# Optimization experiments

Measured on AMD Instinct MI355X. Metric: run time of the kernel, lower is better.

Reference implementation:

```python
import jax, jax.numpy as jnp
import numpy as np

N_NODES = 50000
N_EDGES = 600000
IN_DIM, HID, OUT_DIM = 128, 128, 64
LN_EPS = 1e-5


def setup_inputs() -> dict:
    key = jax.random.key(0)
    ks = jax.random.split(key, 10)
    def glorot(k, shape):
        lim = np.sqrt(6.0 / (shape[0] + shape[1]))
        return jax.random.uniform(k, shape, jnp.float32, -lim, lim)
    return {
        "x": jax.random.normal(ks[0], (N_NODES, IN_DIM), jnp.float32),
        "src": jax.random.randint(ks[1], (N_EDGES,), 0, N_NODES, jnp.int32),
        "dst": jax.random.randint(ks[2], (N_EDGES,), 0, N_NODES, jnp.int32),
        "W0": glorot(ks[3], (IN_DIM, HID)), "b0": jnp.zeros((HID,), jnp.float32),
        "W1": glorot(ks[4], (HID, HID)),    "b1": jnp.zeros((HID,), jnp.float32),
        "W2": glorot(ks[5], (HID, OUT_DIM)),"b2": jnp.zeros((OUT_DIM,), jnp.float32),
        "ln_scale": jnp.ones((HID,), jnp.float32),
        "ln_bias": jnp.zeros((HID,), jnp.float32),
    }


def _degree_norms(src, dst):
    ones = jnp.ones((src.shape[0],), jnp.float32)
    deg_out = jax.ops.segment_sum(ones, src, num_segments=N_NODES)
    deg_in = jax.ops.segment_sum(ones, dst, num_segments=N_NODES)
    # DGL clamps degree to min 1 for norm='both'
    out_norm = jnp.clip(deg_out, 1.0, None) ** -0.5
    in_norm = jnp.clip(deg_in, 1.0, None) ** -0.5
    return out_norm, in_norm


def _graph_conv(h, src, dst, out_norm, in_norm, W, b):
    # norm='both': scale src side, SpMM aggregate, scale dst side, then affine
    h = h * out_norm[:, None]
    h = h @ W  # apply weight first (mathematically identical, smaller messages when out<in)
    agg = jax.ops.segment_sum(h[src], dst, num_segments=N_NODES)  # [N, D]
    return agg * in_norm[:, None] + b


def _layernorm(h, scale, bias):
    mu = jnp.mean(h, axis=-1, keepdims=True)
    var = jnp.var(h, axis=-1, keepdims=True)
    return (h - mu) * jax.lax.rsqrt(var + LN_EPS) * scale + bias


def reference(x, src, dst, W0, b0, W1, b1, W2, b2, ln_scale, ln_bias):
    out_norm, in_norm = _degree_norms(src, dst)
    # dropout is identity in eval mode
    h = jax.nn.relu(_graph_conv(x, src, dst, out_norm, in_norm, W0, b0))
    h = _layernorm(h, ln_scale, ln_bias)
    h = jax.nn.relu(_graph_conv(h, src, dst, out_norm, in_norm, W1, b1))
    h = _layernorm(h, ln_scale, ln_bias)
    # last layer: encoding=True -> keep activation; no norm after last layer
    h = jax.nn.relu(_graph_conv(h, src, dst, out_norm, in_norm, W2, b2))
    return h
```

## Files before the change

kernel.cpp:

```cpp
#include <hip/hip_runtime.h>
#include <hip/hip_fp16.h>

#define NN 50000
#define NE 600000
#define LN_EPS 1e-5f
#define SCAN_B 49
#define RANGES 8
#define RSZ 6250
#define CHUNKS 16
#define CSZ 37500

typedef __attribute__((ext_vector_type(8))) _Float16 half8;
typedef __attribute__((ext_vector_type(4))) float floatx4;

__device__ __align__(16) __half g_h0[NN * 128];
__device__ __align__(16) __half g_h1[NN * 128];
__device__ __align__(16) int g_deg_in[NN];
__device__ float g_out_norm[NN];
__device__ float g_in_norm[NN];
__device__ int g_rowptr[NN + 1];
__device__ int g_esrc[NE];
__device__ int g_blocksum[SCAN_B];
__device__ int g_blockoff[SCAN_B];
__device__ int g_pout[CHUNKS * NN];
__device__ int g_pin[CHUNKS * NN];
__device__ int g_base[CHUNKS * NN];

__device__ __forceinline__ __half* hbuf(int i) { return i ? g_h1 : g_h0; }

__global__ __launch_bounds__(256) void histo_kernel(const int* __restrict__ src,
                                                    const int* __restrict__ dst) {
    __shared__ int h_out[RSZ];
    __shared__ int h_in[RSZ];
    int c = blockIdx.x / RANGES, r = blockIdx.x % RANGES;
    int lo = r * RSZ;
    for (int i = threadIdx.x; i < RSZ; i += 256) { h_out[i] = 0; h_in[i] = 0; }
    __syncthreads();
    const int4* s4 = (const int4*)(src + c * CSZ);
    const int4* d4 = (const int4*)(dst + c * CSZ);
    for (int i = threadIdx.x; i < CSZ / 4; i += 256) {
        int4 s = s4[i], d = d4[i];
        int v;
        v = s.x - lo; if ((unsigned)v < RSZ) atomicAdd(&h_out[v], 1);
        v = s.y - lo; if ((unsigned)v < RSZ) atomicAdd(&h_out[v], 1);
        v = s.z - lo; if ((unsigned)v < RSZ) atomicAdd(&h_out[v], 1);
        v = s.w - lo; if ((unsigned)v < RSZ) atomicAdd(&h_out[v], 1);
        v = d.x - lo; if ((unsigned)v < RSZ) atomicAdd(&h_in[v], 1);
        v = d.y - lo; if ((unsigned)v < RSZ) atomicAdd(&h_in[v], 1);
        v = d.z - lo; if ((unsigned)v < RSZ) atomicAdd(&h_in[v], 1);
        v = d.w - lo; if ((unsigned)v < RSZ) atomicAdd(&h_in[v], 1);
    }
    __syncthreads();
    for (int i = threadIdx.x; i < RSZ; i += 256) {
        g_pout[c * NN + lo + i] = h_out[i];
        g_pin[c * NN + lo + i]  = h_in[i];
    }
}

__global__ __launch_bounds__(1024) void deg_scan1_kernel() {
    __shared__ int wsum[16];
    int b = blockIdx.x, t = threadIdx.x;
    int n = b * 1024 + t;
    int si = 0;
    if (n < NN) {
        int so = 0;
#pragma unroll
        for (int c = 0; c < CHUNKS; ++c) { so += g_pout[c * NN + n]; si += g_pin[c * NN + n]; }
        g_deg_in[n] = si;
        g_out_norm[n] = rsqrtf((float)max(so, 1));
        g_in_norm[n]  = rsqrtf((float)max(si, 1));
    }
    int s = si;
#pragma unroll
    for (int off = 32; off; off >>= 1) s += __shfl_xor(s, off, 64);
    if ((t & 63) == 0) wsum[t >> 6] = s;
    __syncthreads();
    if (t < 16) {
        int v = wsum[t];
#pragma unroll
        for (int off = 8; off; off >>= 1) v += __shfl_xor(v, off, 16);
        if (t == 0) g_blocksum[b] = v;
    }
}

__global__ __launch_bounds__(64) void scan_phase2() {
    int lane = threadIdx.x;
    int own = (lane < SCAN_B) ? g_blocksum[lane] : 0;
    int v = own;
#pragma unroll
    for (int off = 1; off < 64; off <<= 1) {
        int n = __shfl_up(v, off, 64);
        if (lane >= off) v += n;
    }
    if (lane < SCAN_B) g_blockoff[lane] = v - own;
    if (lane == SCAN_B - 1) g_rowptr[NN] = v;
}

__global__ __launch_bounds__(256) void scan3_base_kernel() {
    __shared__ int sums[256];
    int b = blockIdx.x, t = threadIdx.x;
    int base = b * 1024 + t * 4;
    int v[4];
#pragma unroll
    for (int k = 0; k < 4; ++k) v[k] = (base + k < NN) ? g_deg_in[base + k] : 0;
    int tsum = v[0] + v[1] + v[2] + v[3];
    sums[t] = tsum;
    __syncthreads();
    for (int off = 1; off < 256; off <<= 1) {
        int add = (t >= off) ? sums[t - off] : 0;
        __syncthreads();
        sums[t] += add;
        __syncthreads();
    }
    int excl = sums[t] - tsum + g_blockoff[b];
#pragma unroll
    for (int k = 0; k < 4; ++k) {
        int idx = base + k;
        if (idx < NN) {
            g_rowptr[idx] = excl;
            int run = excl;
#pragma unroll
            for (int c = 0; c < CHUNKS; ++c) {
                g_base[c * NN + idx] = run;
                run += g_pin[c * NN + idx];
            }
        }
        excl += v[k];
    }
}

__global__ __launch_bounds__(256) void place_lds_kernel(const int* __restrict__ src,
                                                        const int* __restrict__ dst) {
    __shared__ int cur[RSZ];
    int c = blockIdx.x / RANGES, r = blockIdx.x % RANGES;
    int lo = r * RSZ;
    for (int i = threadIdx.x; i < RSZ; i += 256) cur[i] = g_base[c * NN + lo + i];
    __syncthreads();
    const int4* s4 = (const int4*)(src + c * CSZ);
    const int4* d4 = (const int4*)(dst + c * CSZ);
    for (int i = threadIdx.x; i < CSZ / 4; i += 256) {
        int4 s = s4[i], d = d4[i];
        int v, p;
        v = d.x - lo; if ((unsigned)v < RSZ) { p = atomicAdd(&cur[v], 1); g_esrc[p] = s.x; }
        v = d.y - lo; if ((unsigned)v < RSZ) { p = atomicAdd(&cur[v], 1); g_esrc[p] = s.y; }
        v = d.z - lo; if ((unsigned)v < RSZ) { p = atomicAdd(&cur[v], 1); g_esrc[p] = s.z; }
        v = d.w - lo; if ((unsigned)v < RSZ) { p = atomicAdd(&cur[v], 1); g_esrc[p] = s.w; }
    }
}

template <int N, bool AEXT>
__global__ __launch_bounds__(256) void gemm_mfma(const float* __restrict__ Aext,
                                                 int a_ib, int c_ib,
                                                 const float* __restrict__ Wg,
                                                 int M) {
    constexpr int NT = N / 16;
    constexpr int LOGN = (N == 128) ? 7 : 6;
    __shared__ _Float16 Wl[128 * N];

    const int tid = threadIdx.x;
    for (int e = tid; e < 128 * N; e += 256) {
        int k = e >> LOGN, n = e & (N - 1);
        Wl[(((k >> 3) * N + n) << 3) + (k & 7)] = (_Float16)Wg[e];
    }
    __syncthreads();

    const int wv = tid >> 6, lane = tid & 63;
    const int quad = lane >> 4, mrow = lane & 15;
    const int rowbase = blockIdx.x * 64 + wv * 16;
    const int arow0 = rowbase + mrow;
    const int arow = (arow0 < M) ? arow0 : (M - 1);

    floatx4 acc[NT] = {};
    const __half* Ah = AEXT ? nullptr : hbuf(a_ib);

#pragma unroll
    for (int kk = 0; kk < 4; ++kk) {
        const int k0 = kk * 32 + quad * 8;
        half8 afrag;
        if (AEXT) {
            const float4* ap = (const float4*)(Aext + (size_t)arow * 128 + k0);
            float4 f0 = ap[0], f1 = ap[1];
            afrag[0] = (_Float16)f0.x; afrag[1] = (_Float16)f0.y;
            afrag[2] = (_Float16)f0.z; afrag[3] = (_Float16)f0.w;
            afrag[4] = (_Float16)f1.x; afrag[5] = (_Float16)f1.y;
            afrag[6] = (_Float16)f1.z; afrag[7] = (_Float16)f1.w;
        } else {
            afrag = *(const half8*)(Ah + (size_t)arow * 128 + k0);
        }
#pragma unroll
        for (int nt = 0; nt < NT; ++nt) {
            half8 bfrag = *(const half8*)&Wl[(((kk * 4 + quad) * N + nt * 16 + mrow) << 3)];
            acc[nt] = __builtin_amdgcn_mfma_f32_16x16x32_f16(afrag, bfrag, acc[nt], 0, 0, 0);
        }
    }

    __half* C = hbuf(c_ib);
#pragma unroll
    for (int r = 0; r < 4; ++r) {
        int crow = rowbase + quad * 4 + r;
        if (crow < M) {
            float s = g_out_norm[crow];
#pragma unroll
            for (int nt = 0; nt < NT; ++nt) {
                float v = acc[nt][r] * s;
                C[(size_t)crow * N + nt * 16 + mrow] = __float2half_rn(v);
            }
        }
    }
}

__global__ __launch_bounds__(256) void gather_ln_kernel(int s_ib, int d_ib,
                                                        const float* __restrict__ b,
                                                        const float* __restrict__ ln_s,
                                                        const float* __restrict__ ln_b) {
    int wave = threadIdx.x >> 6;
    int lane = threadIdx.x & 63;
    int sub = lane >> 5, sl = lane & 31;
    int node = blockIdx.x * 8 + wave * 2 + sub;
    const uint2* Hu = (const uint2*)hbuf(s_ib);
    int beg = g_rowptr[node], end = g_rowptr[node + 1];
    float a0 = 0.f, a1 = 0.f, a2 = 0.f, a3 = 0.f;
    int j = beg;
    for (; j + 3 < end; j += 4) {
        int s0 = g_esrc[j], s1 = g_esrc[j + 1], s2 = g_esrc[j + 2], s3 = g_esrc[j + 3];
        uint2 u0 = Hu[s0 * 32 + sl];
        uint2 u1 = Hu[s1 * 32 + sl];
        uint2 u2 = Hu[s2 * 32 + sl];
        uint2 u3 = Hu[s3 * 32 + sl];
        float2 p0 = __half22float2(*(const __half2*)&u0.x), q0 = __half22float2(*(const __half2*)&u0.y);
        float2 p1 = __half22float2(*(const __half2*)&u1.x), q1 = __half22float2(*(const __half2*)&u1.y);
        float2 p2 = __half22float2(*(const __half2*)&u2.x), q2 = __half22float2(*(const __half2*)&u2.y);
        float2 p3 = __half22float2(*(const __half2*)&u3.x), q3 = __half22float2(*(const __half2*)&u3.y);
        a0 += (p0.x + p1.x) + (p2.x + p3.x);
        a1 += (p0.y + p1.y) + (p2.y + p3.y);
        a2 += (q0.x + q1.x) + (q2.x + q3.x);
        a3 += (q0.y + q1.y) + (q2.y + q3.y);
    }
    for (; j < end; ++j) {
        uint2 u = Hu[g_esrc[j] * 32 + sl];
        float2 p = __half22float2(*(const __half2*)&u.x), q = __half22float2(*(const __half2*)&u.y);
        a0 += p.x; a1 += p.y; a2 += q.x; a3 += q.y;
    }
    float nrm = g_in_norm[node];
    float4 bb = ((const float4*)b)[sl];
    float v0 = fmaxf(a0 * nrm + bb.x, 0.f);
    float v1 = fmaxf(a1 * nrm + bb.y, 0.f);
    float v2 = fmaxf(a2 * nrm + bb.z, 0.f);
    float v3 = fmaxf(a3 * nrm + bb.w, 0.f);
    float s = (v0 + v1) + (v2 + v3);
    float sq = (v0 * v0 + v1 * v1) + (v2 * v2 + v3 * v3);
#pragma unroll
    for (int off = 16; off > 0; off >>= 1) {
        s  += __shfl_xor(s, off, 64);
        sq += __shfl_xor(sq, off, 64);
    }
    float mean = s * (1.f / 128.f);
    float var = sq * (1.f / 128.f) - mean * mean;
    float inv = rsqrtf(var + LN_EPS);
    float4 ls = ((const float4*)ln_s)[sl];
    float4 lb = ((const float4*)ln_b)[sl];
    float o0 = (v0 - mean) * inv * ls.x + lb.x;
    float o1 = (v1 - mean) * inv * ls.y + lb.y;
    float o2 = (v2 - mean) * inv * ls.z + lb.z;
    float o3 = (v3 - mean) * inv * ls.w + lb.w;
    __half2 h0 = __floats2half2_rn(o0, o1);
    __half2 h1 = __floats2half2_rn(o2, o3);
    uint2 o = make_uint2(*(const unsigned int*)&h0, *(const unsigned int*)&h1);
    ((uint2*)hbuf(d_ib))[node * 32 + sl] = o;
}

__global__ __launch_bounds__(256) void GCN_63831803953156_kernel(int s_ib,
                                                                 const float* __restrict__ b2,
                                                                 float* __restrict__ out) {
    int wave = threadIdx.x >> 6;
    int lane = threadIdx.x & 63;
    int sub = lane >> 4, sl = lane & 15;
    int node = blockIdx.x * 16 + wave * 4 + sub;
    const uint2* Hu = (const uint2*)hbuf(s_ib);
    int beg = g_rowptr[node], end = g_rowptr[node + 1];
    float a0 = 0.f, a1 = 0.f, a2 = 0.f, a3 = 0.f;
    int j = beg;
    for (; j + 3 < end; j += 4) {
        int s0 = g_esrc[j], s1 = g_esrc[j + 1], s2 = g_esrc[j + 2], s3 = g_esrc[j + 3];
        uint2 u0 = Hu[s0 * 16 + sl];
        uint2 u1 = Hu[s1 * 16 + sl];
        uint2 u2 = Hu[s2 * 16 + sl];
        uint2 u3 = Hu[s3 * 16 + sl];
        float2 p0 = __half22float2(*(const __half2*)&u0.x), q0 = __half22float2(*(const __half2*)&u0.y);
        float2 p1 = __half22float2(*(const __half2*)&u1.x), q1 = __half22float2(*(const __half2*)&u1.y);
        float2 p2 = __half22float2(*(const __half2*)&u2.x), q2 = __half22float2(*(const __half2*)&u2.y);
        float2 p3 = __half22float2(*(const __half2*)&u3.x), q3 = __half22float2(*(const __half2*)&u3.y);
        a0 += (p0.x + p1.x) + (p2.x + p3.x);
        a1 += (p0.y + p1.y) + (p2.y + p3.y);
        a2 += (q0.x + q1.x) + (q2.x + q3.x);
        a3 += (q0.y + q1.y) + (q2.y + q3.y);
    }
    for (; j < end; ++j) {
        uint2 u = Hu[g_esrc[j] * 16 + sl];
        float2 p = __half22float2(*(const __half2*)&u.x), q = __half22float2(*(const __half2*)&u.y);
        a0 += p.x; a1 += p.y; a2 += q.x; a3 += q.y;
    }
    float nrm = g_in_norm[node];
    float4 bb = ((const float4*)b2)[sl];
    float4 o;
    o.x = fmaxf(a0 * nrm + bb.x, 0.f);
    o.y = fmaxf(a1 * nrm + bb.y, 0.f);
    o.z = fmaxf(a2 * nrm + bb.z, 0.f);
    o.w = fmaxf(a3 * nrm + bb.w, 0.f);
    ((float4*)out)[node * 16 + sl] = o;
}

extern "C" void kernel_launch(void* const* d_in, const int* in_sizes, int n_in,
                              void* d_out, int out_size, void* d_ws, size_t ws_size,
                              hipStream_t stream) {
    const float* x   = (const float*)d_in[0];
    const int* src   = (const int*)d_in[1];
    const int* dst   = (const int*)d_in[2];
    const float* W0  = (const float*)d_in[3];
    const float* b0  = (const float*)d_in[4];
    const float* W1  = (const float*)d_in[5];
    const float* b1  = (const float*)d_in[6];
    const float* W2  = (const float*)d_in[7];
    const float* b2  = (const float*)d_in[8];
    const float* ln_s = (const float*)d_in[9];
    const float* ln_b = (const float*)d_in[10];
    (void)d_ws; (void)ws_size; (void)in_sizes; (void)n_in; (void)out_size;

    histo_kernel<<<CHUNKS * RANGES, 256, 0, stream>>>(src, dst);
    deg_scan1_kernel<<<SCAN_B, 1024, 0, stream>>>();
    scan_phase2<<<1, 64, 0, stream>>>();
    scan3_base_kernel<<<SCAN_B, 256, 0, stream>>>();
    place_lds_kernel<<<CHUNKS * RANGES, 256, 0, stream>>>(src, dst);

    const int GB = (NN + 63) / 64;

    gemm_mfma<128, true><<<GB, 256, 0, stream>>>(x, -1, 0, W0, NN);
    gather_ln_kernel<<<NN / 8, 256, 0, stream>>>(0, 1, b0, ln_s, ln_b);

    gemm_mfma<128, false><<<GB, 256, 0, stream>>>(nullptr, 1, 0, W1, NN);
    gather_ln_kernel<<<NN / 8, 256, 0, stream>>>(0, 1, b1, ln_s, ln_b);

    gemm_mfma<64, false><<<GB, 256, 0, stream>>>(nullptr, 1, 0, W2, NN);
    GCN_63831803953156_kernel<<<NN / 16, 256, 0, stream>>>(0, b2, (float*)d_out);
}
```

Measured before the change: 267.2 us.

## Fuse GCN layers into persistent megakernel with software grid barriers

Replaces the six per-layer GEMM and gather launches with one persistent kernel of 391 blocks that loops over tiles and synchronises phases through an atomic grid barrier. The three scan kernels are also merged into one kernel that uses the same barrier. The aim is to remove kernel launch gaps and tail effects between small phases. In exchange, each phase runs on far fewer blocks, which lowers occupancy and latency hiding for the gather-bound phases. The barrier also relies on every block being co-resident, or it can deadlock.

```diff
diff --git a/kernel.cpp b/kernel.cpp
--- a/kernel.cpp
+++ b/kernel.cpp
@@ -9,24 +9,45 @@
 #define RSZ 6250
 #define CHUNKS 16
 #define CSZ 37500
+#define MEGA_GRID 391
 
 typedef __attribute__((ext_vector_type(8))) _Float16 half8;
 typedef __attribute__((ext_vector_type(4))) float floatx4;
 
 __device__ __align__(16) __half g_h0[NN * 128];
 __device__ __align__(16) __half g_h1[NN * 128];
-__device__ __align__(16) int g_deg_in[NN];
 __device__ float g_out_norm[NN];
 __device__ float g_in_norm[NN];
 __device__ int g_rowptr[NN + 1];
 __device__ int g_esrc[NE];
 __device__ int g_blocksum[SCAN_B];
-__device__ int g_blockoff[SCAN_B];
 __device__ int g_pout[CHUNKS * NN];
 __device__ int g_pin[CHUNKS * NN];
 __device__ int g_base[CHUNKS * NN];
+__device__ unsigned g_bar_count = 0;
+__device__ unsigned g_bar_gen = 0;
 
 __device__ __forceinline__ __half* hbuf(int i) { return i ? g_h1 : g_h0; }
+
+__device__ __forceinline__ void gridbar(unsigned* expected) {
+    __syncthreads();
+    if (threadIdx.x == 0) {
+        __threadfence();
+        unsigned prev = __hip_atomic_fetch_add(&g_bar_count, 1u, __ATOMIC_ACQ_REL,
+                                               __HIP_MEMORY_SCOPE_AGENT);
+        if (prev == gridDim.x - 1) {
+            __hip_atomic_store(&g_bar_count, 0u, __ATOMIC_RELAXED, __HIP_MEMORY_SCOPE_AGENT);
+            __hip_atomic_fetch_add(&g_bar_gen, 1u, __ATOMIC_RELEASE, __HIP_MEMORY_SCOPE_AGENT);
+        } else {
+            while (__hip_atomic_load(&g_bar_gen, __ATOMIC_ACQUIRE, __HIP_MEMORY_SCOPE_AGENT) ==
+                   *expected)
+                __builtin_amdgcn_s_sleep(8);
+        }
+        __threadfence();
+    }
+    __syncthreads();
+    (*expected)++;
+}
 
 __global__ __launch_bounds__(256) void histo_kernel(const int* __restrict__ src,
                                                     const int* __restrict__ dst) {
@@ -57,8 +78,10 @@
     }
 }
 
-__global__ __launch_bounds__(1024) void deg_scan1_kernel() {
-    __shared__ int wsum[16];
+__global__ __launch_bounds__(1024) void mid_kernel() {
+    __shared__ int sums[1024];
+    __shared__ int aux[64];
+    unsigned expected = __hip_atomic_load(&g_bar_gen, __ATOMIC_RELAXED, __HIP_MEMORY_SCOPE_AGENT);
     int b = blockIdx.x, t = threadIdx.x;
     int n = b * 1024 + t;
     int si = 0;
@@ -66,66 +89,51 @@
         int so = 0;
 #pragma unroll
         for (int c = 0; c < CHUNKS; ++c) { so += g_pout[c * NN + n]; si += g_pin[c * NN + n]; }
-        g_deg_in[n] = si;
         g_out_norm[n] = rsqrtf((float)max(so, 1));
         g_in_norm[n]  = rsqrtf((float)max(si, 1));
     }
     int s = si;
 #pragma unroll
     for (int off = 32; off; off >>= 1) s += __shfl_xor(s, off, 64);
-    if ((t & 63) == 0) wsum[t >> 6] = s;
+    if ((t & 63) == 0) aux[t >> 6] = s;
     __syncthreads();
     if (t < 16) {
-        int v = wsum[t];
+        int v = aux[t];
 #pragma unroll
         for (int off = 8; off; off >>= 1) v += __shfl_xor(v, off, 16);
         if (t == 0) g_blocksum[b] = v;
     }
-}
-
-__global__ __launch_bounds__(64) void scan_phase2() {
-    int lane = threadIdx.x;
-    int own = (lane < SCAN_B) ? g_blocksum[lane] : 0;
-    int v = own;
-#pragma unroll
-    for (int off = 1; off < 64; off <<= 1) {
-        int n = __shfl_up(v, off, 64);
-        if (lane >= off) v += n;
-    }
-    if (lane < SCAN_B) g_blockoff[lane] = v - own;
-    if (lane == SCAN_B - 1) g_rowptr[NN] = v;
-}
-
-__global__ __launch_bounds__(256) void scan3_base_kernel() {
-    __shared__ int sums[256];
-    int b = blockIdx.x, t = threadIdx.x;
-    int base = b * 1024 + t * 4;
-    int v[4];
-#pragma unroll
-    for (int k = 0; k < 4; ++k) v[k] = (base + k < NN) ? g_deg_in[base + k] : 0;
-    int tsum = v[0] + v[1] + v[2] + v[3];
-    sums[t] = tsum;
-    __syncthreads();
-    for (int off = 1; off < 256; off <<= 1) {
+    gridbar(&expected);
+    if (t < 64) {
+        int own = (t < SCAN_B) ? g_blocksum[t] : 0;
+        int v = own;
+#pragma unroll
+        for (int off = 1; off < 64; off <<= 1) {
+            int nb = __shfl_up(v, off, 64);
+            if (t >= off) v += nb;
+        }
+        aux[t] = v - own;
+        if (b == 0 && t == SCAN_B - 1) g_rowptr[NN] = v;
+    }
+    __syncthreads();
+    int blockoff = aux[b];
+    sums[t] = si;
+    __syncthreads();
+    for (int off = 1; off < 1024; off <<= 1) {
         int add = (t >= off) ? sums[t - off] : 0;
         __syncthreads();
         sums[t] += add;
         __syncthreads();
     }
-    int excl = sums[t] - tsum + g_blockoff[b];
-#pragma unroll
-    for (int k = 0; k < 4; ++k) {
-        int idx = base + k;
-        if (idx < NN) {
-            g_rowptr[idx] = excl;
-            int run = excl;
-#pragma unroll
-            for (int c = 0; c < CHUNKS; ++c) {
-                g_base[c * NN + idx] = run;
-                run += g_pin[c * NN + idx];
-            }
-        }
-        excl += v[k];
+    int excl = sums[t] - si + blockoff;
+    if (n < NN) {
+        g_rowptr[n] = excl;
+        int run = excl;
+#pragma unroll
+        for (int c = 0; c < CHUNKS; ++c) {
+            g_base[c * NN + n] = run;
+            run += g_pin[c * NN + n];
+        }
     }
 }
 
@@ -149,14 +157,10 @@
 }
 
 template <int N, bool AEXT>
-__global__ __launch_bounds__(256) void gemm_mfma(const float* __restrict__ Aext,
-                                                 int a_ib, int c_ib,
-                                                 const float* __restrict__ Wg,
-                                                 int M) {
+__device__ __forceinline__ void gemm_phase(_Float16* Wl, const float* Aext, int a_ib, int c_ib,
+                                           const float* __restrict__ Wg) {
     constexpr int NT = N / 16;
     constexpr int LOGN = (N == 128) ? 7 : 6;
-    __shared__ _Float16 Wl[128 * N];
-
     const int tid = threadIdx.x;
     for (int e = tid; e < 128 * N; e += 256) {
         int k = e >> LOGN, n = e & (N - 1);
@@ -166,148 +170,176 @@
 
     const int wv = tid >> 6, lane = tid & 63;
     const int quad = lane >> 4, mrow = lane & 15;
-    const int rowbase = blockIdx.x * 64 + wv * 16;
-    const int arow0 = rowbase + mrow;
-    const int arow = (arow0 < M) ? arow0 : (M - 1);
-
-    floatx4 acc[NT] = {};
     const __half* Ah = AEXT ? nullptr : hbuf(a_ib);
-
-#pragma unroll
-    for (int kk = 0; kk < 4; ++kk) {
-        const int k0 = kk * 32 + quad * 8;
-        half8 afrag;
-        if (AEXT) {
-            const float4* ap = (const float4*)(Aext + (size_t)arow * 128 + k0);
-            float4 f0 = ap[0], f1 = ap[1];
-            afrag[0] = (_Float16)f0.x; afrag[1] = (_Float16)f0.y;
-            afrag[2] = (_Float16)f0.z; afrag[3] = (_Float16)f0.w;
-            afrag[4] = (_Float16)f1.x; afrag[5] = (_Float16)f1.y;
-            afrag[6] = (_Float16)f1.z; afrag[7] = (_Float16)f1.w;
-        } else {
-            afrag = *(const half8*)(Ah + (size_t)arow * 128 + k0);
-        }
-#pragma unroll
-        for (int nt = 0; nt < NT; ++nt) {
-            half8 bfrag = *(const half8*)&Wl[(((kk * 4 + quad) * N + nt * 16 + mrow) << 3)];
-            acc[nt] = __builtin_amdgcn_mfma_f32_16x16x32_f16(afrag, bfrag, acc[nt], 0, 0, 0);
-        }
-    }
-
     __half* C = hbuf(c_ib);
-#pragma unroll
-    for (int r = 0; r < 4; ++r) {
-        int crow = rowbase + quad * 4 + r;
-        if (crow < M) {
-            float s = g_out_norm[crow];
+    constexpr int NTILES = (NN + 63) / 64;
+
+    for (int tile = blockIdx.x; tile < NTILES; tile += MEGA_GRID) {
+        const int rowbase = tile * 64 + wv * 16;
+        const int arow0 = rowbase + mrow;
+        const int arow = (arow0 < NN) ? arow0 : (NN - 1);
+        floatx4 acc[NT] = {};
+#pragma unroll
+        for (int kk = 0; kk < 4; ++kk) {
+            const int k0 = kk * 32 + quad * 8;
+            half8 afrag;
+            if (AEXT) {
+                const float4* ap = (const float4*)(Aext + (size_t)arow * 128 + k0);
+                float4 f0 = ap[0], f1 = ap[1];
+                afrag[0] = (_Float16)f0.x; afrag[1] = (_Float16)f0.y;
+                afrag[2] = (_Float16)f0.z; afrag[3] = (_Float16)f0.w;
+                afrag[4] = (_Float16)f1.x; afrag[5] = (_Float16)f1.y;
+                afrag[6] = (_Float16)f1.z; afrag[7] = (_Float16)f1.w;
+            } else {
+                afrag = *(const half8*)(Ah + (size_t)arow * 128 + k0);
+            }
 #pragma unroll
             for (int nt = 0; nt < NT; ++nt) {
-                float v = acc[nt][r] * s;
-                C[(size_t)crow * N + nt * 16 + mrow] = __float2half_rn(v);
+                half8 bfrag = *(const half8*)&Wl[(((kk * 4 + quad) * N + nt * 16 + mrow) << 3)];
+                acc[nt] = __builtin_amdgcn_mfma_f32_16x16x32_f16(afrag, bfrag, acc[nt], 0, 0, 0);
             }
         }
-    }
-}
-
-__global__ __launch_bounds__(256) void gather_ln_kernel(int s_ib, int d_ib,
-                                                        const float* __restrict__ b,
-                                                        const float* __restrict__ ln_s,
-                                                        const float* __restrict__ ln_b) {
+#pragma unroll
+        for (int r = 0; r < 4; ++r) {
+            int crow = rowbase + quad * 4 + r;
+            if (crow < NN) {
+                float sc = g_out_norm[crow];
+#pragma unroll
+                for (int nt = 0; nt < NT; ++nt) {
+                    float v = acc[nt][r] * sc;
+                    C[(size_t)crow * N + nt * 16 + mrow] = __float2half_rn(v);
+                }
+            }
+        }
+    }
+}
+
+__device__ __forceinline__ void gather_ln_phase(int s_ib, int d_ib,
+                                                const float* __restrict__ b,
+                                                const float* __restrict__ ln_s,
+                                                const float* __restrict__ ln_b) {
     int wave = threadIdx.x >> 6;
     int lane = threadIdx.x & 63;
     int sub = lane >> 5, sl = lane & 31;
-    int node = blockIdx.x * 8 + wave * 2 + sub;
     const uint2* Hu = (const uint2*)hbuf(s_ib);
-    int beg = g_rowptr[node], end = g_rowptr[node + 1];
-    float a0 = 0.f, a1 = 0.f, a2 = 0.f, a3 = 0.f;
-    int j = beg;
-    for (; j + 3 < end; j += 4) {
-        int s0 = g_esrc[j], s1 = g_esrc[j + 1], s2 = g_esrc[j + 2], s3 = g_esrc[j + 3];
-        uint2 u0 = Hu[s0 * 32 + sl];
-        uint2 u1 = Hu[s1 * 32 + sl];
-        uint2 u2 = Hu[s2 * 32 + sl];
-        uint2 u3 = Hu[s3 * 32 + sl];
-        float2 p0 = __half22float2(*(const __half2*)&u0.x), q0 = __half22float2(*(const __half2*)&u0.y);
-        float2 p1 = __half22float2(*(const __half2*)&u1.x), q1 = __half22float2(*(const __half2*)&u1.y);
-        float2 p2 = __half22float2(*(const __half2*)&u2.x), q2 = __half22float2(*(const __half2*)&u2.y);
-        float2 p3 = __half22float2(*(const __half2*)&u3.x), q3 = __half22float2(*(const __half2*)&u3.y);
-        a0 += (p0.x + p1.x) + (p2.x + p3.x);
-        a1 += (p0.y + p1.y) + (p2.y + p3.y);
-        a2 += (q0.x + q1.x) + (q2.x + q3.x);
-        a3 += (q0.y + q1.y) + (q2.y + q3.y);
-    }
-    for (; j < end; ++j) {
-        uint2 u = Hu[g_esrc[j] * 32 + sl];
-        float2 p = __half22float2(*(const __half2*)&u.x), q = __half22float2(*(const __half2*)&u.y);
-        a0 += p.x; a1 += p.y; a2 += q.x; a3 += q.y;
-    }
-    float nrm = g_in_norm[node];
+    uint2* D = (uint2*)hbuf(d_ib);
     float4 bb = ((const float4*)b)[sl];
-    float v0 = fmaxf(a0 * nrm + bb.x, 0.f);
-    float v1 = fmaxf(a1 * nrm + bb.y, 0.f);
-    float v2 = fmaxf(a2 * nrm + bb.z, 0.f);
-    float v3 = fmaxf(a3 * nrm + bb.w, 0.f);
-    float s = (v0 + v1) + (v2 + v3);
-    float sq = (v0 * v0 + v1 * v1) + (v2 * v2 + v3 * v3);
-#pragma unroll
-    for (int off = 16; off > 0; off >>= 1) {
-        s  += __shfl_xor(s, off, 64);
-        sq += __shfl_xor(sq, off, 64);
-    }
-    float mean = s * (1.f / 128.f);
-    float var = sq * (1.f / 128.f) - mean * mean;
-    float inv = rsqrtf(var + LN_EPS);
     float4 ls = ((const float4*)ln_s)[sl];
     float4 lb = ((const float4*)ln_b)[sl];
-    float o0 = (v0 - mean) * inv * ls.x + lb.x;
-    float o1 = (v1 - mean) * inv * ls.y + lb.y;
-    float o2 = (v2 - mean) * inv * ls.z + lb.z;
-    float o3 = (v3 - mean) * inv * ls.w + lb.w;
-    __half2 h0 = __floats2half2_rn(o0, o1);
-    __half2 h1 = __floats2half2_rn(o2, o3);
-    uint2 o = make_uint2(*(const unsigned int*)&h0, *(const unsigned int*)&h1);
-    ((uint2*)hbuf(d_ib))[node * 32 + sl] = o;
-}
-
-__global__ __launch_bounds__(256) void GCN_63831803953156_kernel(int s_ib,
-                                                                 const float* __restrict__ b2,
-                                                                 float* __restrict__ out) {
+    for (int g = blockIdx.x; g < NN / 8; g += MEGA_GRID) {
+        int node = g * 8 + wave * 2 + sub;
+        int beg = g_rowptr[node], end = g_rowptr[node + 1];
+        float a0 = 0.f, a1 = 0.f, a2 = 0.f, a3 = 0.f;
+        int j = beg;
+        for (; j + 3 < end; j += 4) {
+            int s0 = g_esrc[j], s1 = g_esrc[j + 1], s2 = g_esrc[j + 2], s3 = g_esrc[j + 3];
+            uint2 u0 = Hu[s0 * 32 + sl];
+            uint2 u1 = Hu[s1 * 32 + sl];
+            uint2 u2 = Hu[s2 * 32 + sl];
+            uint2 u3 = Hu[s3 * 32 + sl];
+            float2 p0 = __half22float2(*(const __half2*)&u0.x), q0 = __half22float2(*(const __half2*)&u0.y);
+            float2 p1 = __half22float2(*(const __half2*)&u1.x), q1 = __half22float2(*(const __half2*)&u1.y);
+            float2 p2 = __half22float2(*(const __half2*)&u2.x), q2 = __half22float2(*(const __half2*)&u2.y);
+            float2 p3 = __half22float2(*(const __half2*)&u3.x), q3 = __half22float2(*(const __half2*)&u3.y);
+            a0 += (p0.x + p1.x) + (p2.x + p3.x);
+            a1 += (p0.y + p1.y) + (p2.y + p3.y);
+            a2 += (q0.x + q1.x) + (q2.x + q3.x);
+            a3 += (q0.y + q1.y) + (q2.y + q3.y);
+        }
+        for (; j < end; ++j) {
+            uint2 u = Hu[g_esrc[j] * 32 + sl];
+            float2 p = __half22float2(*(const __half2*)&u.x), q = __half22float2(*(const __half2*)&u.y);
+            a0 += p.x; a1 += p.y; a2 += q.x; a3 += q.y;
+        }
+        float nrm = g_in_norm[node];
+        float v0 = fmaxf(a0 * nrm + bb.x, 0.f);
+        float v1 = fmaxf(a1 * nrm + bb.y, 0.f);
+        float v2 = fmaxf(a2 * nrm + bb.z, 0.f);
+        float v3 = fmaxf(a3 * nrm + bb.w, 0.f);
+        float s = (v0 + v1) + (v2 + v3);
+        float sq = (v0 * v0 + v1 * v1) + (v2 * v2 + v3 * v3);
+#pragma unroll
+        for (int off = 16; off > 0; off >>= 1) {
+            s  += __shfl_xor(s, off, 64);
+            sq += __shfl_xor(sq, off, 64);
+        }
+        float mean = s * (1.f / 128.f);
+        float var = sq * (1.f / 128.f) - mean * mean;
+        float inv = rsqrtf(var + LN_EPS);
+        float o0 = (v0 - mean) * inv * ls.x + lb.x;
+        float o1 = (v1 - mean) * inv * ls.y + lb.y;
+        float o2 = (v2 - mean) * inv * ls.z + lb.z;
+        float o3 = (v3 - mean) * inv * ls.w + lb.w;
+        __half2 h0 = __floats2half2_rn(o0, o1);
+        __half2 h1 = __floats2half2_rn(o2, o3);
+        uint2 o = make_uint2(*(const unsigned int*)&h0, *(const unsigned int*)&h1);
+        D[node * 32 + sl] = o;
+    }
+}
+
+__device__ __forceinline__ void final_phase(int s_ib, const float* __restrict__ b2,
+                                            float* __restrict__ out) {
     int wave = threadIdx.x >> 6;
     int lane = threadIdx.x & 63;
     int sub = lane >> 4, sl = lane & 15;
-    int node = blockIdx.x * 16 + wave * 4 + sub;
     const uint2* Hu = (const uint2*)hbuf(s_ib);
-    int beg = g_rowptr[node], end = g_rowptr[node + 1];
-    float a0 = 0.f, a1 = 0.f, a2 = 0.f, a3 = 0.f;
-    int j = beg;
-    for (; j + 3 < end; j += 4) {
-        int s0 = g_esrc[j], s1 = g_esrc[j + 1], s2 = g_esrc[j + 2], s3 = g_esrc[j + 3];
-        uint2 u0 = Hu[s0 * 16 + sl];
-        uint2 u1 = Hu[s1 * 16 + sl];
-        uint2 u2 = Hu[s2 * 16 + sl];
-        uint2 u3 = Hu[s3 * 16 + sl];
-        float2 p0 = __half22float2(*(const __half2*)&u0.x), q0 = __half22float2(*(const __half2*)&u0.y);
-        float2 p1 = __half22float2(*(const __half2*)&u1.x), q1 = __half22float2(*(const __half2*)&u1.y);
-        float2 p2 = __half22float2(*(const __half2*)&u2.x), q2 = __half22float2(*(const __half2*)&u2.y);
-        float2 p3 = __half22float2(*(const __half2*)&u3.x), q3 = __half22float2(*(const __half2*)&u3.y);
-        a0 += (p0.x + p1.x) + (p2.x + p3.x);
-        a1 += (p0.y + p1.y) + (p2.y + p3.y);
-        a2 += (q0.x + q1.x) + (q2.x + q3.x);
-        a3 += (q0.y + q1.y) + (q2.y + q3.y);
-    }
-    for (; j < end; ++j) {
-        uint2 u = Hu[g_esrc[j] * 16 + sl];
-        float2 p = __half22float2(*(const __half2*)&u.x), q = __half22float2(*(const __half2*)&u.y);
-        a0 += p.x; a1 += p.y; a2 += q.x; a3 += q.y;
-    }
-    float nrm = g_in_norm[node];
     float4 bb = ((const float4*)b2)[sl];
-    float4 o;
-    o.x = fmaxf(a0 * nrm + bb.x, 0.f);
-    o.y = fmaxf(a1 * nrm + bb.y, 0.f);
-    o.z = fmaxf(a2 * nrm + bb.z, 0.f);
-    o.w = fmaxf(a3 * nrm + bb.w, 0.f);
-    ((float4*)out)[node * 16 + sl] = o;
+    for (int g = blockIdx.x; g < NN / 16; g += MEGA_GRID) {
+        int node = g * 16 + wave * 4 + sub;
+        int beg = g_rowptr[node], end = g_rowptr[node + 1];
+        float a0 = 0.f, a1 = 0.f, a2 = 0.f, a3 = 0.f;
+        int j = beg;
+        for (; j + 3 < end; j += 4) {
+            int s0 = g_esrc[j], s1 = g_esrc[j + 1], s2 = g_esrc[j + 2], s3 = g_esrc[j + 3];
+            uint2 u0 = Hu[s0 * 16 + sl];
+            uint2 u1 = Hu[s1 * 16 + sl];
+            uint2 u2 = Hu[s2 * 16 + sl];
+            uint2 u3 = Hu[s3 * 16 + sl];
+            float2 p0 = __half22float2(*(const __half2*)&u0.x), q0 = __half22float2(*(const __half2*)&u0.y);
+            float2 p1 = __half22float2(*(const __half2*)&u1.x), q1 = __half22float2(*(const __half2*)&u1.y);
+            float2 p2 = __half22float2(*(const __half2*)&u2.x), q2 = __half22float2(*(const __half2*)&u2.y);
+            float2 p3 = __half22float2(*(const __half2*)&u3.x), q3 = __half22float2(*(const __half2*)&u3.y);
+            a0 += (p0.x + p1.x) + (p2.x + p3.x);
+            a1 += (p0.y + p1.y) + (p2.y + p3.y);
+            a2 += (q0.x + q1.x) + (q2.x + q3.x);
+            a3 += (q0.y + q1.y) + (q2.y + q3.y);
+        }
+        for (; j < end; ++j) {
+            uint2 u = Hu[g_esrc[j] * 16 + sl];
+            float2 p = __half22float2(*(const __half2*)&u.x), q = __half22float2(*(const __half2*)&u.y);
+            a0 += p.x; a1 += p.y; a2 += q.x; a3 += q.y;
+        }
+        float nrm = g_in_norm[node];
+        float4 o;
+        o.x = fmaxf(a0 * nrm + bb.x, 0.f);
+        o.y = fmaxf(a1 * nrm + bb.y, 0.f);
+        o.z = fmaxf(a2 * nrm + bb.z, 0.f);
+        o.w = fmaxf(a3 * nrm + bb.w, 0.f);
+        ((float4*)out)[node * 16 + sl] = o;
+    }
+}
+
+__global__ __launch_bounds__(256, 2) void GCN_63831803953156_kernel(
+        const float* __restrict__ x,
+        const float* __restrict__ W0, const float* __restrict__ b0,
+        const float* __restrict__ W1, const float* __restrict__ b1,
+        const float* __restrict__ W2, const float* __restrict__ b2,
+        const float* __restrict__ ln_s, const float* __restrict__ ln_b,
+        float* __restrict__ out) {
+    __shared__ __align__(16) _Float16 Wl[128 * 128];
+    unsigned expected = __hip_atomic_load(&g_bar_gen, __ATOMIC_RELAXED, __HIP_MEMORY_SCOPE_AGENT);
+
+    gemm_phase<128, true>(Wl, x, -1, 0, W0);
+    gridbar(&expected);
+    gather_ln_phase(0, 1, b0, ln_s, ln_b);
+    gridbar(&expected);
+    gemm_phase<128, false>(Wl, nullptr, 1, 0, W1);
+    gridbar(&expected);
+    gather_ln_phase(0, 1, b1, ln_s, ln_b);
+    gridbar(&expected);
+    gemm_phase<64, false>(Wl, nullptr, 1, 0, W2);
+    gridbar(&expected);
+    final_phase(0, b2, out);
 }
 
 extern "C" void kernel_launch(void* const* d_in, const int* in_sizes, int n_in,
@@ -327,19 +359,8 @@
     (void)d_ws; (void)ws_size; (void)in_sizes; (void)n_in; (void)out_size;
 
     histo_kernel<<<CHUNKS * RANGES, 256, 0, stream>>>(src, dst);
-    deg_scan1_kernel<<<SCAN_B, 1024, 0, stream>>>();
-    scan_phase2<<<1, 64, 0, stream>>>();
-    scan3_base_kernel<<<SCAN_B, 256, 0, stream>>>();
+    mid_kernel<<<SCAN_B, 1024, 0, stream>>>();
     place_lds_kernel<<<CHUNKS * RANGES, 256, 0, stream>>>(src, dst);
-
-    const int GB = (NN + 63) / 64;
-
-    gemm_mfma<128, true><<<GB, 256, 0, stream>>>(x, -1, 0, W0, NN);
-    gather_ln_kernel<<<NN / 8, 256, 0, stream>>>(0, 1, b0, ln_s, ln_b);
-
-    gemm_mfma<128, false><<<GB, 256, 0, stream>>>(nullptr, 1, 0, W1, NN);
-    gather_ln_kernel<<<NN / 8, 256, 0, stream>>>(0, 1, b1, ln_s, ln_b);
-
-    gemm_mfma<64, false><<<GB, 256, 0, stream>>>(nullptr, 1, 0, W2, NN);
-    GCN_63831803953156_kernel<<<NN / 16, 256, 0, stream>>>(0, b2, (float*)d_out);
-}
+    GCN_63831803953156_kernel<<<MEGA_GRID, 256, 0, stream>>>(x, W0, b0, W1, b1, W2, b2,
+                                                             ln_s, ln_b, (float*)d_out);
+}
```

New measurement: 806.3 us. +201.8%, slower.
